# Kernel optimization log

Hardware: AMD Instinct MI355X
Metric: run time of the kernel (lower is better)

Reference implementation:

```python
import jax, jax.numpy as jnp
import numpy as np

N = 4096        # nodes
E = 65536       # edges (avg degree 16)
L = 64          # latent_dims
K = 256         # kernel_dims
ED = 6          # edge_dims
DEPTH = 2


def _gelu(x):
    # torch.nn.GELU / F.gelu default = exact erf form
    return jax.nn.gelu(x, approximate=False)


def setup_inputs() -> dict:
    key = jax.random.key(0)
    ks = jax.random.split(key, 12)
    u = lambda k, shape, fan: jax.random.uniform(k, shape, jnp.float32, -1.0, 1.0) / np.sqrt(fan)
    return {
        "nodes": jax.random.normal(ks[0], (N, L), jnp.float32),
        "edge_index": jax.random.randint(ks[1], (2, E), 0, N, jnp.int32),
        "edge_attr": jax.random.uniform(ks[2], (E, ED), jnp.float32),
        # DenseNet kernel MLP: ED -> K -> K -> L*L (GELU between layers)
        "W1": u(ks[3], (ED, K), ED), "b1": jnp.zeros((K,), jnp.float32),
        "W2": u(ks[4], (K, K), K),  "b2": jnp.zeros((K,), jnp.float32),
        "W3": u(ks[5], (K, L * L), K), "b3": jnp.zeros((L * L,), jnp.float32),
        # NNConv root linear (no bias) + conv bias
        "W_root": u(ks[6], (L, L), L),
        "bias": jnp.zeros((L,), jnp.float32),
    }


def reference(nodes, edge_index, edge_attr, W1, b1, W2, b2, W3, b3, W_root, bias):
    src, dst = edge_index[0], edge_index[1]
    # Edge-conditioned dynamic weights (depend only on edge_attr -> compute once)
    h = _gelu(edge_attr @ W1 + b1)          # [E, K]
    h = _gelu(h @ W2 + b2)                  # [E, K]
    W_edge = (h @ W3 + b3).reshape(E, L, L) # [E, L_in, L_out]

    def conv(x):
        msg = jnp.einsum('ei,eio->eo', x[src], W_edge)          # gather + per-edge matmul
        agg = jax.ops.segment_sum(msg, dst, num_segments=N)     # scatter-add to dst
        return agg + x @ W_root + bias

    x = nodes
    for idx in range(DEPTH):
        x = conv(x)
        if idx < DEPTH - 1:
            x = _gelu(x)
    return x
```

## Files before the change

### kernel.cpp

```cpp
#include <hip/hip_runtime.h>
#include <math.h>

#define NN 4096
#define NE 65536
#define LL 64
#define KK 256
#define ED 6
#define MAXSUPER 6144

typedef __bf16 bf16_t;
typedef __attribute__((ext_vector_type(4))) __bf16 bf16x4;
typedef __attribute__((ext_vector_type(8))) __bf16 bf16x8;
typedef __attribute__((ext_vector_type(4))) float f32x4;
typedef __attribute__((ext_vector_type(16))) float f32x16;

#define OFF_CNT    ((size_t)0)
#define OFF_DESC   ((size_t)16384)
#define OFF_AGG0   ((size_t)147456)
#define OFF_AGG1   ((size_t)1196032)
#define ZERO_BYTES ((size_t)2244608)
#define OFF_CURSOR ((size_t)2244608)
#define OFF_DSTS   ((size_t)2260992)
#define OFF_W2R    ((size_t)2785280)
#define OFF_W3RR   ((size_t)2916352)
#define OFF_Q0     ((size_t)5013504)
#define OFF_Q1     ((size_t)6062080)
#define OFF_X1F    ((size_t)7110656)
#define OFF_X0BF   ((size_t)8159232)
#define OFF_X1BF   ((size_t)8683520)
#define OFF_H      ((size_t)9207808)

__device__ __forceinline__ float gelu_f(float x) {
    return 0.5f * x * (1.0f + erff(x * 0.7071067811865476f));
}
__device__ __forceinline__ bf16_t f2bf(float x) { return (bf16_t)x; }

__global__ void k_hist(const int* __restrict__ ei, int* __restrict__ cnt) {
    int e = blockIdx.x * 256 + threadIdx.x;
    atomicAdd(&cnt[ei[e]], 1);
}

__global__ void k_scan(const int* __restrict__ cnt, int* __restrict__ cursor,
                       int4* __restrict__ descs) {
    __shared__ int pd[1024], pc[1024];
    int t = threadIdx.x;
    int deg[4]; int sd = 0, sc = 0;
#pragma unroll
    for (int j = 0; j < 4; j++) {
        deg[j] = cnt[t * 4 + j];
        sd += deg[j];
        sc += (deg[j] + 31) >> 5;
    }
    pd[t] = sd; pc[t] = sc;
    __syncthreads();
    for (int off = 1; off < 1024; off <<= 1) {
        int vd = 0, vc = 0;
        if (t >= off) { vd = pd[t - off]; vc = pc[t - off]; }
        __syncthreads();
        pd[t] += vd; pc[t] += vc;
        __syncthreads();
    }
    int rd = (t > 0) ? pd[t - 1] : 0;
    int rc = (t > 0) ? pc[t - 1] : 0;
    for (int j = 0; j < 4; j++) {
        int v = t * 4 + j, d = deg[j];
        cursor[v] = rd;
        int nch = (d + 31) >> 5;
        for (int c = 0; c < nch; c++) {
            int rem = d - c * 32;
            descs[rc + c] = make_int4(v, rd + c * 32, rem < 32 ? rem : 32, 0);
        }
        rc += nch; rd += d;
    }
}

__global__ void __launch_bounds__(256) k_fuse3(
        const int* __restrict__ ei, int* __restrict__ cursor, int* __restrict__ dsts,
        const float* __restrict__ W3, bf16_t* __restrict__ W3rr,
        const float* __restrict__ W2, bf16_t* __restrict__ W2r,
        const float* __restrict__ attr, const float* __restrict__ W1,
        const float* __restrict__ b1, bf16_t* __restrict__ a1,
        const float* __restrict__ x, const float* __restrict__ b3,
        bf16_t* __restrict__ xbf, float* __restrict__ Q) {
    __shared__ float smem[4096];
    int bid = blockIdx.x, tid = threadIdx.x;
    if (bid < 256) {
        int k0 = bid;
        for (int idx = tid; idx < 4096; idx += 256)
            smem[idx] = W3[(size_t)k0 * 4096 + idx];
        __syncthreads();
        int sbase = (2 * (k0 >> 4)) * 512 + (((k0 >> 3) & 1) * 32) * 8 + (k0 & 7);
#pragma unroll
        for (int m = 0; m < 2; m++) {
            int w = m * 256 + tid;
            int o = w >> 3, ib = w & 7;
            int s = sbase + (o >> 5) * 512 + (o & 31) * 8;
            int f = (s >> 4) * 1024 + (ib >> 2) * 512 + (ib & 3) * 128 + (s & 15) * 8;
            bf16x8 pk;
#pragma unroll
            for (int j = 0; j < 8; j++) pk[j] = f2bf(smem[(ib * 8 + j) * 64 + o]);
            *(bf16x8*)(W3rr + f) = pk;
        }
    } else if (bid < 512) {
        int t = (bid - 256) * 256 + tid;
        int kk = t >> 13, nn = (t >> 9) & 15, lane = (t >> 3) & 63, j = t & 7;
        int k = kk * 32 + (lane >> 4) * 8 + j;
        int n = nn * 16 + (lane & 15);
        W2r[t] = f2bf(W2[k * 256 + n]);
    } else if (bid < 1536) {
        float* sa = smem;
        int* spos = (int*)(smem + 512);
        int e0 = (bid - 512) * 64;
        for (int i = tid; i < 64 * ED; i += 256) sa[i] = attr[(size_t)e0 * ED + i];
        if (tid < 64) {
            int e = e0 + tid;
            int s = ei[e], d = ei[NE + e];
            int p = atomicAdd(&cursor[s], 1);
            dsts[p] = d;
            spos[tid] = p;
        }
        int col4 = (tid & 63) * 4;
        float w[ED][4], bb[4];
#pragma unroll
        for (int j = 0; j < ED; j++)
#pragma unroll
            for (int c = 0; c < 4; c++) w[j][c] = W1[j * 256 + col4 + c];
#pragma unroll
        for (int c = 0; c < 4; c++) bb[c] = b1[col4 + c];
        __syncthreads();
        int esub = tid >> 6;
#pragma unroll 1
        for (int eg = 0; eg < 16; eg++) {
            int el = eg * 4 + esub;
            int pos = spos[el];
            float av[ED];
#pragma unroll
            for (int j = 0; j < ED; j++) av[j] = sa[el * ED + j];
            bf16x4 ov;
#pragma unroll
            for (int c = 0; c < 4; c++) {
                float acc = bb[c];
#pragma unroll
                for (int j = 0; j < ED; j++) acc += av[j] * w[j][c];
                ov[c] = f2bf(gelu_f(acc));
            }
            *(bf16x4*)(a1 + (size_t)pos * 256 + col4) = ov;
        }
    } else {
        int v = (bid - 1536) * 4 + (tid >> 6);
        int o = tid & 63;
        float xv = x[v * 64 + o];
        smem[tid] = xv;
        xbf[v * 64 + o] = f2bf(xv);
        __syncthreads();
        const float* sx = smem + (tid >> 6) * 64;
        float q = 0.0f;
#pragma unroll 8
        for (int i = 0; i < 64; i++) q += sx[i] * b3[i * 64 + o];
        Q[v * 64 + o] = q;
    }
}

__global__ void __launch_bounds__(256) k_mlp2(const bf16_t* a1,
                                              const bf16_t* __restrict__ W2r,
                                              const float* __restrict__ b2,
                                              bf16_t* h) {
    __shared__ bf16_t sB[16384];
    int tid = threadIdx.x;
    int wave = tid >> 6, lane = tid & 63, col = lane & 15, quad = lane >> 4;
    int base = blockIdx.x * 128 + wave * 32;
    bf16x8 a[2][8];
#pragma unroll
    for (int t = 0; t < 2; t++) {
        const bf16_t* arow = a1 + (size_t)(base + t * 16 + col) * 256;
#pragma unroll
        for (int kk = 0; kk < 8; kk++)
            a[t][kk] = *(const bf16x8*)(arow + kk * 32 + quad * 8);
    }
#pragma unroll 1
    for (int p = 0; p < 4; p++) {
#pragma unroll
        for (int it = 0; it < 8; it++) {
            int c = it * 256 + tid;
            int fl = c >> 6;
            int e = (c & 63) * 8;
            int kk = fl >> 2, nnl = fl & 3;
            *(bf16x8*)(sB + fl * 512 + e) =
                *(const bf16x8*)(W2r + (size_t)(kk * 16 + p * 4 + nnl) * 512 + e);
        }
        __syncthreads();
#pragma unroll
        for (int nnl = 0; nnl < 4; nnl++) {
            f32x4 acc0, acc1;
#pragma unroll
            for (int r = 0; r < 4; r++) { acc0[r] = 0.0f; acc1[r] = 0.0f; }
#pragma unroll
            for (int kk = 0; kk < 8; kk++) {
                bf16x8 b = *(const bf16x8*)(sB + (kk * 4 + nnl) * 512 + lane * 8);
                acc0 = __builtin_amdgcn_mfma_f32_16x16x32_bf16(a[0][kk], b, acc0, 0, 0, 0);
                acc1 = __builtin_amdgcn_mfma_f32_16x16x32_bf16(a[1][kk], b, acc1, 0, 0, 0);
            }
            int ncol = (p * 4 + nnl) * 16 + col;
            float bv = b2[ncol];
#pragma unroll
            for (int r = 0; r < 4; r++) {
                int row0 = base + quad * 4 + r;
                h[(size_t)row0 * 256 + ncol] = f2bf(gelu_f(acc0[r] + bv));
                h[(size_t)(row0 + 16) * 256 + ncol] = f2bf(gelu_f(acc1[r] + bv));
            }
        }
        __syncthreads();
    }
}

__global__ void __launch_bounds__(512) k_fagg(const int4* __restrict__ descs,
                                              const int* __restrict__ dsts,
                                              const bf16_t* __restrict__ xbf,
                                              const bf16_t* __restrict__ W3rr,
                                              const bf16_t* __restrict__ h,
                                              const float* __restrict__ Q,
                                              float* __restrict__ agg) {
    __shared__ __align__(16) bf16_t Pls[4][16][264];
    __shared__ int sv[16], sbase[16], scnt[16];
    int tid = threadIdx.x, wave = tid >> 6, lane = tid & 63;
    if (tid < 16) {
        int4 d = descs[blockIdx.x * 16 + tid];
        sv[tid] = d.x; sbase[tid] = d.y; scnt[tid] = d.z;
    }
    __syncthreads();

    int tot = 0;
#pragma unroll
    for (int i = 0; i < 16; i++) tot |= scnt[i];
    if (tot == 0) return;

    int col = lane & 15, quad = lane >> 4;
    int row = lane & 31, khalf = lane >> 5;

    const bf16_t* xr = xbf + (size_t)sv[col] * 64 + quad * 8;
    bf16x8 xa0 = *(const bf16x8*)xr;
    bf16x8 xa1 = *(const bf16x8*)(xr + 32);

    int s0 = wave * 2, s1 = s0 + 1;
    int v0 = sv[s0], v1 = sv[s1];
    int cnt0 = scnt[s0], cnt1 = scnt[s1];
    bool val0 = row < cnt0, val1 = row < cnt1;
    int pos0 = sbase[s0] + (val0 ? row : 0);
    int pos1 = sbase[s1] + (val1 ? row : 0);
    int dst0 = dsts[pos0], dst1 = dsts[pos1];
    const bf16_t* h0 = h + (size_t)pos0 * 256 + khalf * 8;
    const bf16_t* h1 = h + (size_t)pos1 * 256 + khalf * 8;

    bf16x8 zero;
#pragma unroll
    for (int i = 0; i < 8; i++) zero[i] = (bf16_t)0.0f;

    bf16x8 hr0[16], hr1[16];
#pragma unroll
    for (int kt = 0; kt < 16; ++kt) {
        bf16x8 t0 = *(const bf16x8*)(h0 + kt * 16);
        bf16x8 t1 = *(const bf16x8*)(h1 + kt * 16);
        hr0[kt] = val0 ? t0 : zero;
        hr1[kt] = val1 ? t1 : zero;
    }

    f32x16 acc00, acc01, acc10, acc11;
#pragma unroll
    for (int r = 0; r < 16; r++) { acc00[r] = 0.0f; acc01[r] = 0.0f;
                                   acc10[r] = 0.0f; acc11[r] = 0.0f; }

    int pst = wave >> 1;
    int nn0 = (wave & 1) * 8;

#pragma unroll
    for (int kt = 0; kt < 16; ++kt) {
        int strip = kt * 4 + pst;
        const bf16_t* wb = W3rr + (size_t)(strip * 16 + nn0) * 1024 + lane * 8;
#pragma unroll
        for (int nn = 0; nn < 8; ++nn) {
            bf16x8 b0 = *(const bf16x8*)wb;
            bf16x8 b1 = *(const bf16x8*)(wb + 512);
            wb += 1024;
            f32x4 acc;
#pragma unroll
            for (int r = 0; r < 4; r++) acc[r] = 0.0f;
            acc = __builtin_amdgcn_mfma_f32_16x16x32_bf16(b0, xa0, acc, 0, 0, 0);
            acc = __builtin_amdgcn_mfma_f32_16x16x32_bf16(b1, xa1, acc, 0, 0, 0);
            bf16x4 pk;
#pragma unroll
            for (int r = 0; r < 4; r++) pk[r] = f2bf(acc[r]);
            *(bf16x4*)(&Pls[pst][col][(nn0 + nn) * 16 + quad * 4]) = pk;
        }
        __syncthreads();
        {
            bf16x8 pb0 = *(const bf16x8*)(&Pls[khalf][s0][row * 8]);
            bf16x8 pb1 = *(const bf16x8*)(&Pls[2 + khalf][s0][row * 8]);
            acc00 = __builtin_amdgcn_mfma_f32_32x32x16_bf16(hr0[kt], pb0, acc00, 0, 0, 0);
            acc01 = __builtin_amdgcn_mfma_f32_32x32x16_bf16(hr0[kt], pb1, acc01, 0, 0, 0);
        }
        {
            bf16x8 pb0 = *(const bf16x8*)(&Pls[khalf][s1][row * 8]);
            bf16x8 pb1 = *(const bf16x8*)(&Pls[2 + khalf][s1][row * 8]);
            acc10 = __builtin_amdgcn_mfma_f32_32x32x16_bf16(hr1[kt], pb0, acc10, 0, 0, 0);
            acc11 = __builtin_amdgcn_mfma_f32_32x32x16_bf16(hr1[kt], pb1, acc11, 0, 0, 0);
        }
        __syncthreads();
    }

    {
        float q0 = Q[v0 * 64 + row];
        float q1 = Q[v0 * 64 + 32 + row];
#pragma unroll
        for (int r = 0; r < 16; r++) {
            int mm = (r & 3) + 8 * (r >> 2) + 4 * khalf;
            int de = __shfl(dst0, mm, 64);
            if (mm < cnt0) {
                atomicAdd(&agg[(size_t)de * 64 + row], acc00[r] + q0);
                atomicAdd(&agg[(size_t)de * 64 + 32 + row], acc01[r] + q1);
            }
        }
    }
    {
        float q0 = Q[v1 * 64 + row];
        float q1 = Q[v1 * 64 + 32 + row];
#pragma unroll
        for (int r = 0; r < 16; r++) {
            int mm = (r & 3) + 8 * (r >> 2) + 4 * khalf;
            int de = __shfl(dst1, mm, 64);
            if (mm < cnt1) {
                atomicAdd(&agg[(size_t)de * 64 + row], acc10[r] + q0);
                atomicAdd(&agg[(size_t)de * 64 + 32 + row], acc11[r] + q1);
            }
        }
    }
}

__global__ void k_combine1(const float* __restrict__ x, const float* __restrict__ agg,
                           const float* __restrict__ Wroot, const float* __restrict__ bias,
                           const float* __restrict__ b3, float* __restrict__ x1,
                           bf16_t* __restrict__ x1bf, float* __restrict__ Q1) {
    __shared__ float sx[64], sy[64];
    int v = blockIdx.x, o = threadIdx.x;
    sx[o] = x[v * 64 + o];
    __syncthreads();
    float acc = agg[v * 64 + o] + bias[o];
#pragma unroll 8
    for (int i = 0; i < 64; i++) acc += sx[i] * Wroot[i * 64 + o];
    acc = gelu_f(acc);
    x1[v * 64 + o] = acc;
    x1bf[v * 64 + o] = f2bf(acc);
    sy[o] = acc;
    __syncthreads();
    float q = 0.0f;
#pragma unroll 8
    for (int i = 0; i < 64; i++) q += sy[i] * b3[i * 64 + o];
    Q1[v * 64 + o] = q;
}

__global__ void k_combine2(const float* __restrict__ x1, const float* __restrict__ agg,
                           const float* __restrict__ Wroot, const float* __restrict__ bias,
                           float* __restrict__ out) {
    __shared__ float sx[64];
    int v = blockIdx.x, o = threadIdx.x;
    sx[o] = x1[v * 64 + o];
    __syncthreads();
    float acc = agg[v * 64 + o] + bias[o];
#pragma unroll 8
    for (int i = 0; i < 64; i++) acc += sx[i] * Wroot[i * 64 + o];
    out[v * 64 + o] = acc;
}

extern "C" void kernel_launch(void* const* d_in, const int* in_sizes, int n_in,
                              void* d_out, int out_size, void* d_ws, size_t ws_size,
                              hipStream_t stream) {
    const float* nodes = (const float*)d_in[0];
    const int*   ei    = (const int*)d_in[1];
    const float* attr  = (const float*)d_in[2];
    const float* W1    = (const float*)d_in[3];
    const float* b1    = (const float*)d_in[4];
    const float* W2    = (const float*)d_in[5];
    const float* b2    = (const float*)d_in[6];
    const float* W3    = (const float*)d_in[7];
    const float* b3    = (const float*)d_in[8];
    const float* Wroot = (const float*)d_in[9];
    const float* bias  = (const float*)d_in[10];
    float* out = (float*)d_out;
    char* ws = (char*)d_ws;

    int*    cnt    = (int*)(ws + OFF_CNT);
    int4*   descs  = (int4*)(ws + OFF_DESC);
    float*  agg0   = (float*)(ws + OFF_AGG0);
    float*  agg1   = (float*)(ws + OFF_AGG1);
    int*    cursor = (int*)(ws + OFF_CURSOR);
    int*    dsts   = (int*)(ws + OFF_DSTS);
    bf16_t* W2r    = (bf16_t*)(ws + OFF_W2R);
    bf16_t* W3rr   = (bf16_t*)(ws + OFF_W3RR);
    float*  Q0     = (float*)(ws + OFF_Q0);
    float*  Q1     = (float*)(ws + OFF_Q1);
    float*  x1f    = (float*)(ws + OFF_X1F);
    bf16_t* x0bf   = (bf16_t*)(ws + OFF_X0BF);
    bf16_t* x1bf   = (bf16_t*)(ws + OFF_X1BF);
    bf16_t* hbuf   = (bf16_t*)(ws + OFF_H);
    bf16_t* a1buf  = (bf16_t*)(ws + OFF_H);

    hipMemsetAsync(ws, 0, ZERO_BYTES, stream);
    k_hist<<<NE / 256, 256, 0, stream>>>(ei, cnt);
    k_scan<<<1, 1024, 0, stream>>>(cnt, cursor, descs);
    k_fuse3<<<2560, 256, 0, stream>>>(ei, cursor, dsts, W3, W3rr, W2, W2r,
                                      attr, W1, b1, a1buf, nodes, b3, x0bf, Q0);
    k_mlp2<<<512, 256, 0, stream>>>(a1buf, W2r, b2, hbuf);
    k_fagg<<<MAXSUPER / 16, 512, 0, stream>>>(descs, dsts, x0bf, W3rr, hbuf, Q0, agg0);
    k_combine1<<<NN, 64, 0, stream>>>(nodes, agg0, Wroot, bias, b3, x1f, x1bf, Q1);
    k_fagg<<<MAXSUPER / 16, 512, 0, stream>>>(descs, dsts, x1bf, W3rr, hbuf, Q1, agg1);
    k_combine2<<<NN, 64, 0, stream>>>(x1f, agg1, Wroot, bias, out);
}
```

Measured before the change: 287.7 us.

## Process 32 source chunks per fused-aggregation block to reuse W3 loads

Each k_fagg block now handles 32 source-node chunks instead of 16, and each wave handles four chunks instead of two. Every W3 tile loaded from global memory now feeds two projection MFMAs (one per 16-node group), halving W3 traffic per chunk, and the grid shrinks to half as many blocks. The h rows are now loaded per k-step inside a non-unrolled loop instead of being preloaded into registers. This trades register-held h for a higher accumulator register count (eight f32x16 per lane) and fewer blocks, which may lower occupancy or load balance.

```diff
diff --git a/kernel.cpp b/kernel.cpp
--- a/kernel.cpp
+++ b/kernel.cpp
@@ -220,60 +220,64 @@
                                               const bf16_t* __restrict__ h,
                                               const float* __restrict__ Q,
                                               float* __restrict__ agg) {
-    __shared__ __align__(16) bf16_t Pls[4][16][264];
-    __shared__ int sv[16], sbase[16], scnt[16];
+    __shared__ __align__(16) bf16_t Pls[4][32][264];
+    __shared__ int sv[32], sbase[32], scnt[32];
     int tid = threadIdx.x, wave = tid >> 6, lane = tid & 63;
-    if (tid < 16) {
-        int4 d = descs[blockIdx.x * 16 + tid];
+    if (tid < 32) {
+        int4 d = descs[blockIdx.x * 32 + tid];
         sv[tid] = d.x; sbase[tid] = d.y; scnt[tid] = d.z;
     }
     __syncthreads();
 
     int tot = 0;
 #pragma unroll
-    for (int i = 0; i < 16; i++) tot |= scnt[i];
+    for (int i = 0; i < 32; i++) tot |= scnt[i];
     if (tot == 0) return;
 
     int col = lane & 15, quad = lane >> 4;
     int row = lane & 31, khalf = lane >> 5;
 
-    const bf16_t* xr = xbf + (size_t)sv[col] * 64 + quad * 8;
-    bf16x8 xa0 = *(const bf16x8*)xr;
-    bf16x8 xa1 = *(const bf16x8*)(xr + 32);
-
-    int s0 = wave * 2, s1 = s0 + 1;
-    int v0 = sv[s0], v1 = sv[s1];
-    int cnt0 = scnt[s0], cnt1 = scnt[s1];
-    bool val0 = row < cnt0, val1 = row < cnt1;
-    int pos0 = sbase[s0] + (val0 ? row : 0);
-    int pos1 = sbase[s1] + (val1 ? row : 0);
-    int dst0 = dsts[pos0], dst1 = dsts[pos1];
-    const bf16_t* h0 = h + (size_t)pos0 * 256 + khalf * 8;
-    const bf16_t* h1 = h + (size_t)pos1 * 256 + khalf * 8;
+    const bf16_t* xr0 = xbf + (size_t)sv[col] * 64 + quad * 8;
+    const bf16_t* xr1 = xbf + (size_t)sv[16 + col] * 64 + quad * 8;
+    bf16x8 x0a = *(const bf16x8*)xr0;
+    bf16x8 x0b = *(const bf16x8*)(xr0 + 32);
+    bf16x8 x1a = *(const bf16x8*)xr1;
+    bf16x8 x1b = *(const bf16x8*)(xr1 + 32);
+
+    int cs = wave * 4;
+    int vv[4], cc[4], dd[4];
+    bool vl[4];
+    const bf16_t* hp[4];
+#pragma unroll
+    for (int c = 0; c < 4; c++) {
+        vv[c] = sv[cs + c]; cc[c] = scnt[cs + c];
+        vl[c] = row < cc[c];
+        int pos = sbase[cs + c] + (vl[c] ? row : 0);
+        dd[c] = dsts[pos];
+        hp[c] = h + (size_t)pos * 256 + khalf * 8;
+    }
 
     bf16x8 zero;
 #pragma unroll
     for (int i = 0; i < 8; i++) zero[i] = (bf16_t)0.0f;
 
-    bf16x8 hr0[16], hr1[16];
-#pragma unroll
-    for (int kt = 0; kt < 16; ++kt) {
-        bf16x8 t0 = *(const bf16x8*)(h0 + kt * 16);
-        bf16x8 t1 = *(const bf16x8*)(h1 + kt * 16);
-        hr0[kt] = val0 ? t0 : zero;
-        hr1[kt] = val1 ? t1 : zero;
-    }
-
-    f32x16 acc00, acc01, acc10, acc11;
-#pragma unroll
-    for (int r = 0; r < 16; r++) { acc00[r] = 0.0f; acc01[r] = 0.0f;
-                                   acc10[r] = 0.0f; acc11[r] = 0.0f; }
+    f32x16 accA[4], accB[4];
+#pragma unroll
+    for (int c = 0; c < 4; c++)
+#pragma unroll
+        for (int r = 0; r < 16; r++) { accA[c][r] = 0.0f; accB[c][r] = 0.0f; }
 
     int pst = wave >> 1;
     int nn0 = (wave & 1) * 8;
 
-#pragma unroll
+#pragma unroll 1
     for (int kt = 0; kt < 16; ++kt) {
+        bf16x8 hv[4];
+#pragma unroll
+        for (int c = 0; c < 4; c++) {
+            bf16x8 t = *(const bf16x8*)(hp[c] + kt * 16);
+            hv[c] = vl[c] ? t : zero;
+        }
         int strip = kt * 4 + pst;
         const bf16_t* wb = W3rr + (size_t)(strip * 16 + nn0) * 1024 + lane * 8;
 #pragma unroll
@@ -281,55 +285,41 @@
             bf16x8 b0 = *(const bf16x8*)wb;
             bf16x8 b1 = *(const bf16x8*)(wb + 512);
             wb += 1024;
-            f32x4 acc;
-#pragma unroll
-            for (int r = 0; r < 4; r++) acc[r] = 0.0f;
-            acc = __builtin_amdgcn_mfma_f32_16x16x32_bf16(b0, xa0, acc, 0, 0, 0);
-            acc = __builtin_amdgcn_mfma_f32_16x16x32_bf16(b1, xa1, acc, 0, 0, 0);
-            bf16x4 pk;
-#pragma unroll
-            for (int r = 0; r < 4; r++) pk[r] = f2bf(acc[r]);
-            *(bf16x4*)(&Pls[pst][col][(nn0 + nn) * 16 + quad * 4]) = pk;
-        }
-        __syncthreads();
-        {
-            bf16x8 pb0 = *(const bf16x8*)(&Pls[khalf][s0][row * 8]);
-            bf16x8 pb1 = *(const bf16x8*)(&Pls[2 + khalf][s0][row * 8]);
-            acc00 = __builtin_amdgcn_mfma_f32_32x32x16_bf16(hr0[kt], pb0, acc00, 0, 0, 0);
-            acc01 = __builtin_amdgcn_mfma_f32_32x32x16_bf16(hr0[kt], pb1, acc01, 0, 0, 0);
-        }
-        {
-            bf16x8 pb0 = *(const bf16x8*)(&Pls[khalf][s1][row * 8]);
-            bf16x8 pb1 = *(const bf16x8*)(&Pls[2 + khalf][s1][row * 8]);
-            acc10 = __builtin_amdgcn_mfma_f32_32x32x16_bf16(hr1[kt], pb0, acc10, 0, 0, 0);
-            acc11 = __builtin_amdgcn_mfma_f32_32x32x16_bf16(hr1[kt], pb1, acc11, 0, 0, 0);
-        }
-        __syncthreads();
-    }
-
-    {
-        float q0 = Q[v0 * 64 + row];
-        float q1 = Q[v0 * 64 + 32 + row];
+            f32x4 p0, p1;
+#pragma unroll
+            for (int r = 0; r < 4; r++) { p0[r] = 0.0f; p1[r] = 0.0f; }
+            p0 = __builtin_amdgcn_mfma_f32_16x16x32_bf16(b0, x0a, p0, 0, 0, 0);
+            p0 = __builtin_amdgcn_mfma_f32_16x16x32_bf16(b1, x0b, p0, 0, 0, 0);
+            p1 = __builtin_amdgcn_mfma_f32_16x16x32_bf16(b0, x1a, p1, 0, 0, 0);
+            p1 = __builtin_amdgcn_mfma_f32_16x16x32_bf16(b1, x1b, p1, 0, 0, 0);
+            bf16x4 k0, k1;
+#pragma unroll
+            for (int r = 0; r < 4; r++) { k0[r] = f2bf(p0[r]); k1[r] = f2bf(p1[r]); }
+            *(bf16x4*)(&Pls[pst][col][(nn0 + nn) * 16 + quad * 4]) = k0;
+            *(bf16x4*)(&Pls[pst][16 + col][(nn0 + nn) * 16 + quad * 4]) = k1;
+        }
+        __syncthreads();
+#pragma unroll
+        for (int c = 0; c < 4; c++) {
+            bf16x8 pb0 = *(const bf16x8*)(&Pls[khalf][cs + c][row * 8]);
+            bf16x8 pb1 = *(const bf16x8*)(&Pls[2 + khalf][cs + c][row * 8]);
+            accA[c] = __builtin_amdgcn_mfma_f32_32x32x16_bf16(hv[c], pb0, accA[c], 0, 0, 0);
+            accB[c] = __builtin_amdgcn_mfma_f32_32x32x16_bf16(hv[c], pb1, accB[c], 0, 0, 0);
+        }
+        __syncthreads();
+    }
+
+#pragma unroll
+    for (int c = 0; c < 4; c++) {
+        float q0 = Q[vv[c] * 64 + row];
+        float q1 = Q[vv[c] * 64 + 32 + row];
 #pragma unroll
         for (int r = 0; r < 16; r++) {
             int mm = (r & 3) + 8 * (r >> 2) + 4 * khalf;
-            int de = __shfl(dst0, mm, 64);
-            if (mm < cnt0) {
-                atomicAdd(&agg[(size_t)de * 64 + row], acc00[r] + q0);
-                atomicAdd(&agg[(size_t)de * 64 + 32 + row], acc01[r] + q1);
-            }
-        }
-    }
-    {
-        float q0 = Q[v1 * 64 + row];
-        float q1 = Q[v1 * 64 + 32 + row];
-#pragma unroll
-        for (int r = 0; r < 16; r++) {
-            int mm = (r & 3) + 8 * (r >> 2) + 4 * khalf;
-            int de = __shfl(dst1, mm, 64);
-            if (mm < cnt1) {
-                atomicAdd(&agg[(size_t)de * 64 + row], acc10[r] + q0);
-                atomicAdd(&agg[(size_t)de * 64 + 32 + row], acc11[r] + q1);
+            int de = __shfl(dd[c], mm, 64);
+            if (mm < cc[c]) {
+                atomicAdd(&agg[(size_t)de * 64 + row], accA[c][r] + q0);
+                atomicAdd(&agg[(size_t)de * 64 + 32 + row], accB[c][r] + q1);
             }
         }
     }
@@ -409,8 +399,8 @@
     k_fuse3<<<2560, 256, 0, stream>>>(ei, cursor, dsts, W3, W3rr, W2, W2r,
                                       attr, W1, b1, a1buf, nodes, b3, x0bf, Q0);
     k_mlp2<<<512, 256, 0, stream>>>(a1buf, W2r, b2, hbuf);
-    k_fagg<<<MAXSUPER / 16, 512, 0, stream>>>(descs, dsts, x0bf, W3rr, hbuf, Q0, agg0);
+    k_fagg<<<MAXSUPER / 32, 512, 0, stream>>>(descs, dsts, x0bf, W3rr, hbuf, Q0, agg0);
     k_combine1<<<NN, 64, 0, stream>>>(nodes, agg0, Wroot, bias, b3, x1f, x1bf, Q1);
-    k_fagg<<<MAXSUPER / 16, 512, 0, stream>>>(descs, dsts, x1bf, W3rr, hbuf, Q1, agg1);
+    k_fagg<<<MAXSUPER / 32, 512, 0, stream>>>(descs, dsts, x1bf, W3rr, hbuf, Q1, agg1);
     k_combine2<<<NN, 64, 0, stream>>>(x1f, agg1, Wroot, bias, out);
 }
```

Result: slower. 304.7 us (+5.9%).
